# Optimization experiments

Hardware: AMD Instinct MI355X
Metric: run time of the kernel (lower is better)

Reference implementation:

```python
import jax, jax.numpy as jnp
import numpy as np

H_HEADS = 16
STATE_N = 64

def setup_inputs() -> dict:
    key = jax.random.key(0)
    ks = jax.random.split(key, 9)
    B, T, D = 2, 1024, 1024
    H, ch, N = H_HEADS, D // H_HEADS, STATE_N
    inp = jax.random.normal(ks[0], (B, T, D), dtype=jnp.float32)
    # lin_logA params scaled so exp(cumsum(logA)) stays bounded (decaying state)
    W_logA = jax.random.normal(ks[1], (H, 1, ch), dtype=jnp.float32) * 0.01
    b_logA = jnp.full((H, 1), -0.05, dtype=jnp.float32)
    W_XBC = jax.random.normal(ks[3], (H, ch + 2 * N, ch), dtype=jnp.float32) * (1.0 / np.sqrt(ch))
    b_XBC = jax.random.normal(ks[4], (H, ch + 2 * N), dtype=jnp.float32) * 0.02
    W_gate = jax.random.normal(ks[5], (H, ch, ch), dtype=jnp.float32) * (1.0 / np.sqrt(ch))
    b_gate = jax.random.normal(ks[6], (H, ch), dtype=jnp.float32) * 0.02
    W_out = jax.random.normal(ks[7], (D, D), dtype=jnp.float32) * (1.0 / np.sqrt(D))
    b_out = jax.random.normal(ks[8], (D,), dtype=jnp.float32) * 0.02
    return {"inp": inp, "W_logA": W_logA, "b_logA": b_logA, "W_XBC": W_XBC,
            "b_XBC": b_XBC, "W_gate": W_gate, "b_gate": b_gate,
            "W_out": W_out, "b_out": b_out}

def _mamba2_forward(inp, W_logA, b_logA, W_XBC, b_XBC, W_gate, b_gate, W_out, b_out):
    B, T, D = inp.shape
    H, N = H_HEADS, STATE_N
    ch = D // H
    x = inp.reshape(B, T, H, ch)  # B,T,H,ch
    # MultiheadLinear: matmul((H,out,in), x[...,None]) + bias
    logA = jnp.einsum('hoc,bthc->btho', W_logA, x)[..., 0] + b_logA[:, 0]  # B,T,H
    XBC = jax.nn.silu(jnp.einsum('hoc,bthc->btho', W_XBC, x) + b_XBC)     # B,T,H,ch+2N
    X = XBC[..., :ch]                 # B,T,H,ch
    Bm = XBC[..., ch:ch + N]          # B,T,H,N
    Cm = XBC[..., ch + N:]            # B,T,H,N
    # quadratic SSM: A_ss[b,h,i,j] = exp(cum[i]-cum[j]) for j<=i else 0
    cum = jnp.cumsum(jnp.swapaxes(logA, 1, 2), axis=-1)  # B,H,T
    diff = cum[..., :, None] - cum[..., None, :]          # B,H,T,T
    causal = jnp.tril(jnp.ones((T, T), dtype=bool))
    A_ss = jnp.where(causal, jnp.exp(jnp.where(causal, diff, 0.0)), 0.0)  # B,H,T,T
    G = jnp.einsum('bihn,bjhn->bhij', Cm, Bm)             # B,H,T,T (C_i . B_j)
    Y = jnp.einsum('bhij,bjhc->bihc', A_ss * G, X)        # B,T,H,ch
    gate = jnp.einsum('hoc,bthc->btho', W_gate, x) + b_gate
    Yg = (gate * Y).reshape(B, T, D)
    return Yg @ W_out.T + b_out

def reference(inp, W_logA, b_logA, W_XBC, b_XBC, W_gate, b_gate, W_out, b_out):
    return _mamba2_forward(inp, W_logA, b_logA, W_XBC, b_XBC, W_gate, b_gate, W_out, b_out)
```

## Files before the change

### kernel.cpp

```cpp
#include <hip/hip_runtime.h>

typedef unsigned int   u32;
typedef unsigned short u16;
typedef __attribute__((ext_vector_type(8))) short bf16x8;
typedef __attribute__((ext_vector_type(4))) float f32x4;

__device__ __forceinline__ float bfs(u16 u) {
  union { u32 i; float f; } v; v.i = ((u32)u) << 16; return v.f;
}
__device__ __forceinline__ u16 f2bf(float f) {
  union { float f; u32 i; } v; v.f = f;
  u32 r = v.i + 0x7fffu + ((v.i >> 16) & 1u);
  return (u16)(r >> 16);
}
__device__ __forceinline__ ushort4 f2bf4(float4 v) {
  ushort4 p; p.x = f2bf(v.x); p.y = f2bf(v.y); p.z = f2bf(v.z); p.w = f2bf(v.w);
  return p;
}

__global__ __launch_bounds__(256, 2) void k_main(
    const float* __restrict__ inp,
    const float* __restrict__ W_XBC,  const float* __restrict__ b_XBC,
    const float* __restrict__ W_gate, const float* __restrict__ b_gate,
    const float* __restrict__ W_logA, const float* __restrict__ b_logA,
    u32* __restrict__ flags, float* __restrict__ decArr,
    float* __restrict__ G, u16* __restrict__ Yg)
{
  const int tt = blockIdx.x, h = blockIdx.y;
  const int tid = threadIdx.x;
  const int w = tid >> 6, l = tid & 63, q = l >> 4, lr = l & 15;
  const int m0 = tt * 64;
  const int b = tt >> 4;
  const int bh = b * 16 + h;
  const int it = tt & 15;

  __shared__ u16 Xt[64][72];
  __shared__ u16 Wt[256][72];
  __shared__ float wl[64];
  __shared__ float sg[64];
  __shared__ float ref_[64], cef[64];

  if (tid < 64) wl[tid] = W_logA[h * 64 + tid];
#pragma unroll
  for (int i = 0; i < 4; ++i) {
    int f = tid + 256 * i; int r = f >> 4, cq = f & 15;
    float4 xv = *(const float4*)(inp + (size_t)(m0 + r) * 1024 + h * 64 + 4 * cq);
    *(ushort4*)&Xt[r][4 * cq] = f2bf4(xv);
  }
#pragma unroll
  for (int i = 0; i < 16; ++i) {
    int f = tid + 256 * i; int r = f >> 4, cq = f & 15;
    const float* ws = (r < 192) ? (W_XBC + ((size_t)h * 192 + r) * 64)
                                : (W_gate + ((size_t)h * 64 + (r - 192)) * 64);
    *(ushort4*)&Wt[r][4 * cq] = f2bf4(*(const float4*)(ws + 4 * cq));
  }
  __syncthreads();

  {
    bf16x8 af[4][2];
#pragma unroll
    for (int rt = 0; rt < 4; ++rt) {
      af[rt][0] = *(const bf16x8*)&Xt[16 * rt + lr][q * 8];
      af[rt][1] = *(const bf16x8*)&Xt[16 * rt + lr][32 + q * 8];
    }

    f32x4 acc[4][4];
#pragma unroll
    for (int rt = 0; rt < 4; ++rt)
#pragma unroll
      for (int ct = 0; ct < 4; ++ct) acc[rt][ct] = (f32x4){0.f, 0.f, 0.f, 0.f};

#pragma unroll
    for (int ct = 0; ct < 4; ++ct) {
      bf16x8 b0 = *(const bf16x8*)&Wt[64 * w + 16 * ct + lr][q * 8];
      bf16x8 b1 = *(const bf16x8*)&Wt[64 * w + 16 * ct + lr][32 + q * 8];
#pragma unroll
      for (int rt = 0; rt < 4; ++rt) {
        acc[rt][ct] = __builtin_amdgcn_mfma_f32_16x16x32_bf16(af[rt][0], b0, acc[rt][ct], 0, 0, 0);
        acc[rt][ct] = __builtin_amdgcn_mfma_f32_16x16x32_bf16(af[rt][1], b1, acc[rt][ct], 0, 0, 0);
      }
    }

    if (tid < 64) {
      float a = b_logA[h];
#pragma unroll 16
      for (int k = 0; k < 64; ++k) a += bfs(Xt[tid][k]) * wl[k];
      float lv = a;
#pragma unroll
      for (int off = 1; off < 64; off <<= 1) {
        float n = __shfl_up(lv, off, 64);
        if (tid >= off) lv += n;
      }
      float L = __shfl(lv, 63, 64);
      sg[tid]   = __expf(L - lv);
      ref_[tid] = __expf(lv);
      cef[tid]  = __expf(-lv);
      if (tid == 63)
        __hip_atomic_store(&decArr[bh * 16 + it], __expf(L),
                           __ATOMIC_RELAXED, __HIP_MEMORY_SCOPE_AGENT);
    }

    if (w < 3) {
#pragma unroll
      for (int ct = 0; ct < 4; ++ct) {
        float bias = b_XBC[h * 192 + 64 * w + 16 * ct + lr];
#pragma unroll
        for (int rt = 0; rt < 4; ++rt)
#pragma unroll
          for (int r = 0; r < 4; ++r) {
            float s = acc[rt][ct][r] + bias;
            acc[rt][ct][r] = s / (1.f + __expf(-s));
          }
      }
    } else {
#pragma unroll
      for (int ct = 0; ct < 4; ++ct) {
        float bias = b_gate[h * 64 + 16 * ct + lr];
#pragma unroll
        for (int rt = 0; rt < 4; ++rt)
#pragma unroll
          for (int r = 0; r < 4; ++r) acc[rt][ct][r] += bias;
      }
    }
    __syncthreads();

#pragma unroll
    for (int ct = 0; ct < 4; ++ct)
#pragma unroll
      for (int rt = 0; rt < 4; ++rt)
#pragma unroll
        for (int r = 0; r < 4; ++r) {
          int t = 16 * rt + 4 * q + r, n = 16 * ct + lr;
          u16 v = f2bf(acc[rt][ct][r]);
          if (w == 0) {
            Wt[n][t] = v;
          } else if (w == 1) {
            Wt[64 + n][t] = v;
            Xt[t][n] = v;
          } else if (w == 2) {
            Wt[128 + t][n] = v;
          } else {
            Wt[192 + t][n] = v;
          }
        }
    __syncthreads();

    {
      bf16x8 a0r = *(const bf16x8*)&Wt[16 * w + lr][q * 8];
      bf16x8 a1r = *(const bf16x8*)&Wt[16 * w + lr][32 + q * 8];
      bf16x8 a0, a1;
#pragma unroll
      for (int jj = 0; jj < 8; ++jj) {
        a0[jj] = (short)f2bf(bfs((u16)a0r[jj]) * sg[q * 8 + jj]);
        a1[jj] = (short)f2bf(bfs((u16)a1r[jj]) * sg[32 + q * 8 + jj]);
      }
      f32x4 gacc[4];
#pragma unroll
      for (int nt = 0; nt < 4; ++nt) {
        gacc[nt] = (f32x4){0.f, 0.f, 0.f, 0.f};
        bf16x8 bb0 = *(const bf16x8*)&Wt[64 + 16 * nt + lr][q * 8];
        bf16x8 bb1 = *(const bf16x8*)&Wt[64 + 16 * nt + lr][32 + q * 8];
        gacc[nt] = __builtin_amdgcn_mfma_f32_16x16x32_bf16(a0, bb0, gacc[nt], 0, 0, 0);
        gacc[nt] = __builtin_amdgcn_mfma_f32_16x16x32_bf16(a1, bb1, gacc[nt], 0, 0, 0);
      }
      float* Gt = G + ((size_t)bh * 16 + it) * 4096;
#pragma unroll
      for (int nt = 0; nt < 4; ++nt)
#pragma unroll
        for (int r = 0; r < 4; ++r)
          __hip_atomic_store(&Gt[(16 * w + 4 * q + r) * 64 + 16 * nt + lr],
                             gacc[nt][r], __ATOMIC_RELAXED,
                             __HIP_MEMORY_SCOPE_AGENT);
    }
  }

  __syncthreads();
  if (tid == 0)
    __hip_atomic_store(&flags[bh * 16 + it], 1u,
                       __ATOMIC_RELEASE, __HIP_MEMORY_SCOPE_AGENT);

  float hreg[16];
#pragma unroll
  for (int k = 0; k < 16; ++k) hreg[k] = 0.f;

  if (it > 0) {
    if (tid < it) {
      while (__hip_atomic_load(&flags[bh * 16 + tid],
                               __ATOMIC_ACQUIRE, __HIP_MEMORY_SCOPE_AGENT) == 0u)
        __builtin_amdgcn_s_sleep(2);
      wl[tid] = __hip_atomic_load(&decArr[bh * 16 + tid],
                                  __ATOMIC_RELAXED, __HIP_MEMORY_SCOPE_AGENT);
    }
    __syncthreads();

    const float* Gb = G + (size_t)bh * 16 * 4096 + tid * 16;
    for (int j = 0; j < it; ++j) {
      const f32x4* Gj = (const f32x4*)(Gb + (size_t)j * 4096);
      f32x4 g0 = Gj[0];
      f32x4 g1 = Gj[1];
      f32x4 g2 = Gj[2];
      f32x4 g3 = Gj[3];
      float dj = wl[j];
      hreg[0]  = dj * hreg[0]  + g0[0]; hreg[1]  = dj * hreg[1]  + g0[1];
      hreg[2]  = dj * hreg[2]  + g0[2]; hreg[3]  = dj * hreg[3]  + g0[3];
      hreg[4]  = dj * hreg[4]  + g1[0]; hreg[5]  = dj * hreg[5]  + g1[1];
      hreg[6]  = dj * hreg[6]  + g1[2]; hreg[7]  = dj * hreg[7]  + g1[3];
      hreg[8]  = dj * hreg[8]  + g2[0]; hreg[9]  = dj * hreg[9]  + g2[1];
      hreg[10] = dj * hreg[10] + g2[2]; hreg[11] = dj * hreg[11] + g2[3];
      hreg[12] = dj * hreg[12] + g3[0]; hreg[13] = dj * hreg[13] + g3[1];
      hreg[14] = dj * hreg[14] + g3[2]; hreg[15] = dj * hreg[15] + g3[3];
    }
  }

  {
    u16 (*Xts)[72] = (u16 (*)[72])&Wt[0];
    u16 (*Sts)[72] = (u16 (*)[72])&Wt[64];
    u16 (*Cts)[72] = (u16 (*)[72])&Wt[128];
    u16 (*Gts)[72] = (u16 (*)[72])&Wt[192];

    bf16x8 ca0 = *(const bf16x8*)&Cts[16 * w + lr][q * 8];
    bf16x8 ca1 = *(const bf16x8*)&Cts[16 * w + lr][32 + q * 8];

#pragma unroll
    for (int ct = 0; ct < 4; ++ct) {
      f32x4 s = (f32x4){0.f, 0.f, 0.f, 0.f};
      bf16x8 b0 = *(const bf16x8*)&Xt[16 * ct + lr][q * 8];
      bf16x8 b1 = *(const bf16x8*)&Xt[16 * ct + lr][32 + q * 8];
      s = __builtin_amdgcn_mfma_f32_16x16x32_bf16(ca0, b0, s, 0, 0, 0);
      s = __builtin_amdgcn_mfma_f32_16x16x32_bf16(ca1, b1, s, 0, 0, 0);
      int jl = 16 * ct + lr;
      float cj = cef[jl];
#pragma unroll
      for (int r = 0; r < 4; ++r) {
        int il = 16 * w + q * 4 + r;
        float v = (jl > il) ? 0.f : s[r] * ref_[il] * cj;
        Sts[il][jl] = f2bf(v);
      }
    }
    __syncthreads();

    {
      int c = tid >> 2, n0 = (tid & 3) * 16;
#pragma unroll
      for (int g4 = 0; g4 < 4; ++g4) {
        ushort4 hv;
        hv.x = f2bf(hreg[4 * g4 + 0]); hv.y = f2bf(hreg[4 * g4 + 1]);
        hv.z = f2bf(hreg[4 * g4 + 2]); hv.w = f2bf(hreg[4 * g4 + 3]);
        *(ushort4*)&Xt[c][n0 + 4 * g4] = hv;
      }
    }
    __syncthreads();

    bf16x8 sa0 = *(const bf16x8*)&Sts[16 * w + lr][q * 8];
    bf16x8 sa1 = *(const bf16x8*)&Sts[16 * w + lr][32 + q * 8];
    f32x4 accd[4], acco[4];
#pragma unroll
    for (int ct = 0; ct < 4; ++ct) {
      accd[ct] = (f32x4){0.f, 0.f, 0.f, 0.f};
      acco[ct] = (f32x4){0.f, 0.f, 0.f, 0.f};
      bf16x8 x0 = *(const bf16x8*)&Xts[16 * ct + lr][q * 8];
      bf16x8 x1 = *(const bf16x8*)&Xts[16 * ct + lr][32 + q * 8];
      accd[ct] = __builtin_amdgcn_mfma_f32_16x16x32_bf16(sa0, x0, accd[ct], 0, 0, 0);
      accd[ct] = __builtin_amdgcn_mfma_f32_16x16x32_bf16(sa1, x1, accd[ct], 0, 0, 0);
      bf16x8 h0 = *(const bf16x8*)&Xt[16 * ct + lr][q * 8];
      bf16x8 h1 = *(const bf16x8*)&Xt[16 * ct + lr][32 + q * 8];
      acco[ct] = __builtin_amdgcn_mfma_f32_16x16x32_bf16(ca0, h0, acco[ct], 0, 0, 0);
      acco[ct] = __builtin_amdgcn_mfma_f32_16x16x32_bf16(ca1, h1, acco[ct], 0, 0, 0);
    }

    __syncthreads();

#pragma unroll
    for (int ct = 0; ct < 4; ++ct) {
      int c = 16 * ct + lr;
#pragma unroll
      for (int r = 0; r < 4; ++r) {
        int il = 16 * w + q * 4 + r;
        float y = accd[ct][r] + ref_[il] * acco[ct][r];
        Xts[il][c] = f2bf(y);
      }
    }
    __syncthreads();

#pragma unroll
    for (int i = 0; i < 4; ++i) {
      int f = tid + 256 * i; int r = f >> 4, cq = f & 15;
      ushort4 yv = *(ushort4*)&Xts[r][4 * cq];
      ushort4 gv = *(ushort4*)&Gts[r][4 * cq];
      ushort4 o;
      o.x = f2bf(bfs(yv.x) * bfs(gv.x));
      o.y = f2bf(bfs(yv.y) * bfs(gv.y));
      o.z = f2bf(bfs(yv.z) * bfs(gv.z));
      o.w = f2bf(bfs(yv.w) * bfs(gv.w));
      *(ushort4*)(Yg + (size_t)(m0 + r) * 1024 + h * 64 + 4 * cq) = o;
    }
  }
}

__global__ __launch_bounds__(512) void k_out(
    const u16* __restrict__ Yg, const float* __restrict__ Wout,
    const float* __restrict__ bout, float* __restrict__ out)
{
  int bm = blockIdx.x, bn = blockIdx.y;
  int tid = threadIdx.x;
  int w = tid >> 6, l = tid & 63, q = l >> 4, lr = l & 15;
  int m0 = bm * 128, d0 = bn * 64;

  __shared__ u16 Yt[128][72];
  __shared__ u16 Wt[64][72];

  f32x4 acc[4];
#pragma unroll
  for (int ct = 0; ct < 4; ++ct) acc[ct] = (f32x4){0.f, 0.f, 0.f, 0.f};

  ushort4 py[4];
  float4 pwf[2];
#pragma unroll
  for (int i = 0; i < 4; ++i) {
    int f = tid + 512 * i; int r = f >> 4, cq = f & 15;
    py[i] = *(const ushort4*)(Yg + (size_t)(m0 + r) * 1024 + 4 * cq);
  }
#pragma unroll
  for (int i = 0; i < 2; ++i) {
    int f = tid + 512 * i; int r = f >> 4, cq = f & 15;
    pwf[i] = *(const float4*)(Wout + (size_t)(d0 + r) * 1024 + 4 * cq);
  }

  for (int kt = 0; kt < 16; ++kt) {
    __syncthreads();
#pragma unroll
    for (int i = 0; i < 4; ++i) {
      int f = tid + 512 * i; int r = f >> 4, cq = f & 15;
      *(ushort4*)&Yt[r][4 * cq] = py[i];
    }
#pragma unroll
    for (int i = 0; i < 2; ++i) {
      int f = tid + 512 * i; int r = f >> 4, cq = f & 15;
      *(ushort4*)&Wt[r][4 * cq] = f2bf4(pwf[i]);
    }
    __syncthreads();

    if (kt < 15) {
      int k1 = (kt + 1) * 64;
#pragma unroll
      for (int i = 0; i < 4; ++i) {
        int f = tid + 512 * i; int r = f >> 4, cq = f & 15;
        py[i] = *(const ushort4*)(Yg + (size_t)(m0 + r) * 1024 + k1 + 4 * cq);
      }
#pragma unroll
      for (int i = 0; i < 2; ++i) {
        int f = tid + 512 * i; int r = f >> 4, cq = f & 15;
        pwf[i] = *(const float4*)(Wout + (size_t)(d0 + r) * 1024 + k1 + 4 * cq);
      }
    }

    bf16x8 a0 = *(const bf16x8*)&Yt[16 * w + lr][q * 8];
    bf16x8 a1 = *(const bf16x8*)&Yt[16 * w + lr][32 + q * 8];
#pragma unroll
    for (int ct = 0; ct < 4; ++ct) {
      bf16x8 b0 = *(const bf16x8*)&Wt[16 * ct + lr][q * 8];
      bf16x8 b1 = *(const bf16x8*)&Wt[16 * ct + lr][32 + q * 8];
      acc[ct] = __builtin_amdgcn_mfma_f32_16x16x32_bf16(a0, b0, acc[ct], 0, 0, 0);
      acc[ct] = __builtin_amdgcn_mfma_f32_16x16x32_bf16(a1, b1, acc[ct], 0, 0, 0);
    }
  }

#pragma unroll
  for (int ct = 0; ct < 4; ++ct) {
    int d = d0 + 16 * ct + lr;
    float bo = bout[d];
#pragma unroll
    for (int r = 0; r < 4; ++r) {
      int m = m0 + 16 * w + q * 4 + r;
      out[(size_t)m * 1024 + d] = acc[ct][r] + bo;
    }
  }
}

extern "C" void kernel_launch(void* const* d_in, const int* in_sizes, int n_in,
                              void* d_out, int out_size, void* d_ws, size_t ws_size,
                              hipStream_t stream)
{
  const float* inp   = (const float*)d_in[0];
  const float* WlogA = (const float*)d_in[1];
  const float* blogA = (const float*)d_in[2];
  const float* WXBC  = (const float*)d_in[3];
  const float* bXBC  = (const float*)d_in[4];
  const float* Wgate = (const float*)d_in[5];
  const float* bgate = (const float*)d_in[6];
  const float* Wout  = (const float*)d_in[7];
  const float* bout  = (const float*)d_in[8];
  float* out = (float*)d_out;

  u32*   flags = (u32*)d_ws;
  float* decA  = (float*)((char*)d_ws + 2048);
  float* G     = decA + 512;
  u16*   Yg    = (u16*)(G + (size_t)32 * 16 * 4096);

  (void)hipMemsetAsync(flags, 0, 2048, stream);

  k_main<<<dim3(32, 16, 1), dim3(256, 1, 1), 0, stream>>>(
      inp, WXBC, bXBC, Wgate, bgate, WlogA, blogA,
      flags, decA, G, Yg);
  k_out<<<dim3(16, 16, 1), dim3(512, 1, 1), 0, stream>>>(Yg, Wout, bout, out);
}
```

Before: 133.0 us.

## Fuse output projection into main kernel with per-row-tile completion flags

Result: slower. 176.4 us (+32.6%).

```diff
diff --git a/kernel.cpp b/kernel.cpp
--- a/kernel.cpp
+++ b/kernel.cpp
@@ -23,8 +23,10 @@
     const float* __restrict__ W_XBC,  const float* __restrict__ b_XBC,
     const float* __restrict__ W_gate, const float* __restrict__ b_gate,
     const float* __restrict__ W_logA, const float* __restrict__ b_logA,
-    u32* __restrict__ flags, float* __restrict__ decArr,
-    float* __restrict__ G, u16* __restrict__ Yg)
+    const float* __restrict__ Wout,   const float* __restrict__ bout,
+    u32* __restrict__ flags, u32* __restrict__ ytflag,
+    float* __restrict__ decArr, float* __restrict__ G,
+    u16* __restrict__ Yg, float* __restrict__ out)
 {
   const int tt = blockIdx.x, h = blockIdx.y;
   const int tid = threadIdx.x;
@@ -287,92 +289,91 @@
       int f = tid + 256 * i; int r = f >> 4, cq = f & 15;
       ushort4 yv = *(ushort4*)&Xts[r][4 * cq];
       ushort4 gv = *(ushort4*)&Gts[r][4 * cq];
-      ushort4 o;
-      o.x = f2bf(bfs(yv.x) * bfs(gv.x));
-      o.y = f2bf(bfs(yv.y) * bfs(gv.y));
-      o.z = f2bf(bfs(yv.z) * bfs(gv.z));
-      o.w = f2bf(bfs(yv.w) * bfs(gv.w));
-      *(ushort4*)(Yg + (size_t)(m0 + r) * 1024 + h * 64 + 4 * cq) = o;
-    }
-  }
-}
-
-__global__ __launch_bounds__(512) void k_out(
-    const u16* __restrict__ Yg, const float* __restrict__ Wout,
-    const float* __restrict__ bout, float* __restrict__ out)
-{
-  int bm = blockIdx.x, bn = blockIdx.y;
-  int tid = threadIdx.x;
-  int w = tid >> 6, l = tid & 63, q = l >> 4, lr = l & 15;
-  int m0 = bm * 128, d0 = bn * 64;
-
-  __shared__ u16 Yt[128][72];
-  __shared__ u16 Wt[64][72];
-
-  f32x4 acc[4];
-#pragma unroll
-  for (int ct = 0; ct < 4; ++ct) acc[ct] = (f32x4){0.f, 0.f, 0.f, 0.f};
-
-  ushort4 py[4];
-  float4 pwf[2];
-#pragma unroll
-  for (int i = 0; i < 4; ++i) {
-    int f = tid + 512 * i; int r = f >> 4, cq = f & 15;
-    py[i] = *(const ushort4*)(Yg + (size_t)(m0 + r) * 1024 + 4 * cq);
-  }
-#pragma unroll
-  for (int i = 0; i < 2; ++i) {
-    int f = tid + 512 * i; int r = f >> 4, cq = f & 15;
-    pwf[i] = *(const float4*)(Wout + (size_t)(d0 + r) * 1024 + 4 * cq);
-  }
-
-  for (int kt = 0; kt < 16; ++kt) {
-    __syncthreads();
+      u32 lo = (u32)f2bf(bfs(yv.x) * bfs(gv.x))
+             | ((u32)f2bf(bfs(yv.y) * bfs(gv.y)) << 16);
+      u32 hi = (u32)f2bf(bfs(yv.z) * bfs(gv.z))
+             | ((u32)f2bf(bfs(yv.w) * bfs(gv.w)) << 16);
+      u32* dst = (u32*)(Yg + (size_t)(m0 + r) * 1024 + h * 64 + 4 * cq);
+      __hip_atomic_store(dst + 0, lo, __ATOMIC_RELAXED, __HIP_MEMORY_SCOPE_AGENT);
+      __hip_atomic_store(dst + 1, hi, __ATOMIC_RELAXED, __HIP_MEMORY_SCOPE_AGENT);
+    }
+  }
+
+  __syncthreads();
+  if (tid == 0)
+    __hip_atomic_fetch_add(&ytflag[tt], 1u,
+                           __ATOMIC_ACQ_REL, __HIP_MEMORY_SCOPE_AGENT);
+
+  {
+    const int d0 = h * 64;
+    u16 (*Yt)[72]  = Xt;
+    u16 (*Wtt)[72] = (u16 (*)[72])&Wt[0];
+
+    float4 pwf[4];
 #pragma unroll
     for (int i = 0; i < 4; ++i) {
-      int f = tid + 512 * i; int r = f >> 4, cq = f & 15;
-      *(ushort4*)&Yt[r][4 * cq] = py[i];
-    }
-#pragma unroll
-    for (int i = 0; i < 2; ++i) {
-      int f = tid + 512 * i; int r = f >> 4, cq = f & 15;
-      *(ushort4*)&Wt[r][4 * cq] = f2bf4(pwf[i]);
-    }
-    __syncthreads();
-
-    if (kt < 15) {
-      int k1 = (kt + 1) * 64;
+      int f = tid + 256 * i; int r = f >> 4, cq = f & 15;
+      pwf[i] = *(const float4*)(Wout + (size_t)(d0 + r) * 1024 + 4 * cq);
+    }
+
+    if (tid == 0) {
+      while (__hip_atomic_load(&ytflag[tt],
+                               __ATOMIC_ACQUIRE, __HIP_MEMORY_SCOPE_AGENT) < 16u)
+        __builtin_amdgcn_s_sleep(2);
+    }
+    __syncthreads();
+
+    f32x4 oacc[4];
+#pragma unroll
+    for (int ct = 0; ct < 4; ++ct) oacc[ct] = (f32x4){0.f, 0.f, 0.f, 0.f};
+
+    ushort4 py[4];
+#pragma unroll
+    for (int i = 0; i < 4; ++i) {
+      int f = tid + 256 * i; int r = f >> 4, cq = f & 15;
+      py[i] = *(const ushort4*)(Yg + (size_t)(m0 + r) * 1024 + 4 * cq);
+    }
+
+    for (int kt = 0; kt < 16; ++kt) {
+      __syncthreads();
 #pragma unroll
       for (int i = 0; i < 4; ++i) {
-        int f = tid + 512 * i; int r = f >> 4, cq = f & 15;
-        py[i] = *(const ushort4*)(Yg + (size_t)(m0 + r) * 1024 + k1 + 4 * cq);
-      }
-#pragma unroll
-      for (int i = 0; i < 2; ++i) {
-        int f = tid + 512 * i; int r = f >> 4, cq = f & 15;
-        pwf[i] = *(const float4*)(Wout + (size_t)(d0 + r) * 1024 + k1 + 4 * cq);
-      }
-    }
-
-    bf16x8 a0 = *(const bf16x8*)&Yt[16 * w + lr][q * 8];
-    bf16x8 a1 = *(const bf16x8*)&Yt[16 * w + lr][32 + q * 8];
+        int f = tid + 256 * i; int r = f >> 4, cq = f & 15;
+        *(ushort4*)&Yt[r][4 * cq]  = py[i];
+        *(ushort4*)&Wtt[r][4 * cq] = f2bf4(pwf[i]);
+      }
+      __syncthreads();
+
+      if (kt < 15) {
+        int k1 = (kt + 1) * 64;
+#pragma unroll
+        for (int i = 0; i < 4; ++i) {
+          int f = tid + 256 * i; int r = f >> 4, cq = f & 15;
+          py[i]  = *(const ushort4*)(Yg + (size_t)(m0 + r) * 1024 + k1 + 4 * cq);
+          pwf[i] = *(const float4*)(Wout + (size_t)(d0 + r) * 1024 + k1 + 4 * cq);
+        }
+      }
+
+      bf16x8 a0 = *(const bf16x8*)&Yt[16 * w + lr][q * 8];
+      bf16x8 a1 = *(const bf16x8*)&Yt[16 * w + lr][32 + q * 8];
+#pragma unroll
+      for (int ct = 0; ct < 4; ++ct) {
+        bf16x8 b0 = *(const bf16x8*)&Wtt[16 * ct + lr][q * 8];
+        bf16x8 b1 = *(const bf16x8*)&Wtt[16 * ct + lr][32 + q * 8];
+        oacc[ct] = __builtin_amdgcn_mfma_f32_16x16x32_bf16(a0, b0, oacc[ct], 0, 0, 0);
+        oacc[ct] = __builtin_amdgcn_mfma_f32_16x16x32_bf16(a1, b1, oacc[ct], 0, 0, 0);
+      }
+    }
+
 #pragma unroll
     for (int ct = 0; ct < 4; ++ct) {
-      bf16x8 b0 = *(const bf16x8*)&Wt[16 * ct + lr][q * 8];
-      bf16x8 b1 = *(const bf16x8*)&Wt[16 * ct + lr][32 + q * 8];
-      acc[ct] = __builtin_amdgcn_mfma_f32_16x16x32_bf16(a0, b0, acc[ct], 0, 0, 0);
-      acc[ct] = __builtin_amdgcn_mfma_f32_16x16x32_bf16(a1, b1, acc[ct], 0, 0, 0);
-    }
-  }
-
-#pragma unroll
-  for (int ct = 0; ct < 4; ++ct) {
-    int d = d0 + 16 * ct + lr;
-    float bo = bout[d];
-#pragma unroll
-    for (int r = 0; r < 4; ++r) {
-      int m = m0 + 16 * w + q * 4 + r;
-      out[(size_t)m * 1024 + d] = acc[ct][r] + bo;
+      int d = d0 + 16 * ct + lr;
+      float bo = bout[d];
+#pragma unroll
+      for (int r = 0; r < 4; ++r) {
+        int m = m0 + 16 * w + q * 4 + r;
+        out[(size_t)m * 1024 + d] = oacc[ct][r] + bo;
+      }
     }
   }
 }
@@ -392,15 +393,15 @@
   const float* bout  = (const float*)d_in[8];
   float* out = (float*)d_out;
 
-  u32*   flags = (u32*)d_ws;
-  float* decA  = (float*)((char*)d_ws + 2048);
-  float* G     = decA + 512;
-  u16*   Yg    = (u16*)(G + (size_t)32 * 16 * 4096);
-
-  (void)hipMemsetAsync(flags, 0, 2048, stream);
+  u32*   flags  = (u32*)d_ws;
+  u32*   ytflag = (u32*)((char*)d_ws + 2048);
+  float* decA   = (float*)((char*)d_ws + 4096);
+  float* G      = decA + 512;
+  u16*   Yg     = (u16*)(G + (size_t)32 * 16 * 4096);
+
+  (void)hipMemsetAsync(d_ws, 0, 4096, stream);
 
   k_main<<<dim3(32, 16, 1), dim3(256, 1, 1), 0, stream>>>(
-      inp, WXBC, bXBC, Wgate, bgate, WlogA, blogA,
-      flags, decA, G, Yg);
-  k_out<<<dim3(16, 16, 1), dim3(512, 1, 1), 0, stream>>>(Yg, Wout, bout, out);
+      inp, WXBC, bXBC, Wgate, bgate, WlogA, blogA, Wout, bout,
+      flags, ytflag, decA, G, Yg, out);
 }
```
